# Kernel tuning notes

Measured on AMD Instinct MI355X. Metric: run time of the kernel, lower is better.

## Reference

```python
import jax, jax.numpy as jnp
import numpy as np

B, C, H, W, NH = 4, 96, 256, 256, 4


def setup_inputs() -> dict:
    key = jax.random.key(0)
    ks = jax.random.split(key, 8)
    s = 0.05  # keep pre-activations well-scaled
    return {
        "x": jax.random.normal(ks[0], (B, C, H, W), jnp.float32),
        "ff": jax.random.normal(ks[1], (B, C, H, W), jnp.float32),
        "w_q": jax.random.normal(ks[2], (C, C, 1, 1), jnp.float32) * s,
        "w_kv": jax.random.normal(ks[3], (2 * C, C, 1, 1), jnp.float32) * s,
        "w_q_dw": jax.random.normal(ks[4], (C, 1, 3, 3), jnp.float32) * s,
        "w_kv_dw": jax.random.normal(ks[5], (2 * C, 1, 3, 3), jnp.float32) * s,
        "w_out": jax.random.normal(ks[6], (C, C, 1, 1), jnp.float32) * s,
        "temperature": jnp.ones((NH, 1, 1), jnp.float32),
    }


def _conv1x1(x, w):
    # pointwise conv == channel GEMM; w: [O, I, 1, 1]
    return jnp.einsum('bchw,oc->bohw', x, w[:, :, 0, 0])


def _dwconv3(x, w):
    # depthwise 3x3, padding=1; w: [C, 1, 3, 3]
    return jax.lax.conv_general_dilated(
        x, w, window_strides=(1, 1), padding='SAME',
        feature_group_count=x.shape[1],
        dimension_numbers=('NCHW', 'OIHW', 'NCHW'))


def _l2norm(t, eps=1e-12):
    # L2-normalize along last (HW) axis, torch F.normalize semantics
    n = jnp.sqrt(jnp.sum(t * t, axis=-1, keepdims=True))
    return t / jnp.maximum(n, eps)


def reference(x, ff, w_q, w_kv, w_q_dw, w_kv_dw, w_out, temperature):
    b, c, h, w = x.shape
    q = _dwconv3(_conv1x1(ff, w_q), w_q_dw)          # [B,C,H,W]
    kv = _dwconv3(_conv1x1(x, w_kv), w_kv_dw)        # [B,2C,H,W]
    k, v = jnp.split(kv, 2, axis=1)

    def heads(t):
        return t.reshape(b, NH, c // NH, h * w)       # [B,nh,c,HW]

    q = _l2norm(heads(q))
    k = _l2norm(heads(k))
    v = heads(v)
    # channel-wise (transposed) attention: [B,nh,c,c]
    attn = jax.nn.softmax(jnp.einsum('bhcn,bhdn->bhcd', q, k) * temperature, axis=-1)
    o = jnp.einsum('bhcd,bhdn->bhcn', attn, v).reshape(b, c, h, w)
    return _conv1x1(o, w_out)
```

## Files before the change

### kernel.cpp

```cpp
#include <hip/hip_runtime.h>
#include <hip/hip_bf16.h>
#include <hip/hip_fp16.h>

typedef unsigned int u32;
typedef unsigned short u16;
typedef _Float16 f16;

static constexpr int HWn = 65536;

typedef __attribute__((ext_vector_type(8))) f16 f16x8;
typedef __attribute__((ext_vector_type(2))) f16 f16x2;
typedef __attribute__((ext_vector_type(4))) float f32x4;

__device__ __forceinline__ float h2f(u16 u) {
    union { u16 s; f16 h; } z; z.s = u; return (float)z.h;
}
__device__ __forceinline__ u16 f2h(float f) {
    union { u16 s; f16 h; } z; z.h = (f16)f; return z.s;
}
__device__ __forceinline__ u32 pack2h(float a, float b) {
    union { u32 i; f16 h[2]; } z; z.h[0] = (f16)a; z.h[1] = (f16)b; return z.i;
}
__device__ __forceinline__ float hlo(u32 u) {
    union { u32 i; f16 h[2]; } z; z.i = u; return (float)z.h[0];
}
__device__ __forceinline__ float hhi(u32 u) {
    union { u32 i; f16 h[2]; } z; z.i = u; return (float)z.h[1];
}
__device__ __forceinline__ float sq2h(u32 a) {
    const float l = hlo(a), h = hhi(a);
    return fmaf(l, l, h * h);
}

#if defined(__has_builtin)
#if __has_builtin(__builtin_amdgcn_fdot2)
#define HAS_FDOT2 1
#endif
#endif
__device__ __forceinline__ float fdot2a(u32 a, u32 b, float c) {
#ifdef HAS_FDOT2
    union { u32 i; f16x2 h; } A, B; A.i = a; B.i = b;
    return __builtin_amdgcn_fdot2(A.h, B.h, c, false);
#else
    return fmaf(hlo(a), hlo(b), fmaf(hhi(a), hhi(b), c));
#endif
}

__device__ __forceinline__ int xoff(int px, int icb) {
    return px * 128 + (((icb ^ (px & 7) ^ ((px >> 3) & 7))) << 3);
}

__global__ __launch_bounds__(256) void k_prep_w(
    const float* __restrict__ wq, const float* __restrict__ wkv,
    u16* __restrict__ wf)
{
    const int i = blockIdx.x * 256 + threadIdx.x;
    if (i >= 288 * 96) return;
    const int row = i / 96, ic = i % 96;
    const float w = (row < 96) ? wq[row * 96 + ic] : wkv[(row - 96) * 96 + ic];
    wf[i] = f2h(w);
}

__global__ __launch_bounds__(256, 5) void k_conv_mfma(
    const float* __restrict__ ff, const float* __restrict__ x,
    const u16* __restrict__ wf,
    u16* __restrict__ qpre, u16* __restrict__ kvpre)
{
    const int b = blockIdx.z, sec = blockIdx.y;
    const int px0 = blockIdx.x * 128;
    const int tid = threadIdx.x;

    __shared__ __align__(16) u16 xs[16384];

    const float* src = (sec == 0 ? ff : x) + (size_t)b * 96 * HWn;

    const int icq = (tid >> 4) * 2;
    const int pxs = (tid & 15) * 8;
    #pragma unroll 1
    for (int p = 0; p < 3; ++p) {
        const int ic = p * 32 + icq;
        const float* rp0 = src + (size_t)ic * HWn + px0 + pxs;
        const float* rp1 = rp0 + HWn;
        const float4 a0 = *reinterpret_cast<const float4*>(rp0);
        const float4 a1 = *reinterpret_cast<const float4*>(rp0 + 4);
        const float4 b0 = *reinterpret_cast<const float4*>(rp1);
        const float4 b1 = *reinterpret_cast<const float4*>(rp1 + 4);
        const int icb = ic >> 3, icl = ic & 7;
        const float e0[8] = {a0.x, a0.y, a0.z, a0.w, a1.x, a1.y, a1.z, a1.w};
        const float e1[8] = {b0.x, b0.y, b0.z, b0.w, b1.x, b1.y, b1.z, b1.w};
        #pragma unroll
        for (int j = 0; j < 8; ++j) {
            const int o = xoff(pxs + j, icb) + icl;
            *reinterpret_cast<u32*>(&xs[o]) = pack2h(e0[j], e1[j]);
        }
    }
    __syncthreads();

    const int lane = tid & 63;
    const int wv = tid >> 6;
    const int oc0 = (wv >> 1) * 48;
    const int pxw = (wv & 1) * 64;
    const int lr = lane & 15, lg = lane >> 4;

    const int npass = (sec == 0) ? 1 : 2;
    #pragma unroll 1
    for (int kvs = 0; kvs < npass; ++kvs) {
        const u16* wh = wf + ((sec == 0) ? 0 : (96 + kvs * 96)) * 96;
        u16* dst = (sec == 0) ? (qpre + (size_t)b * 96 * HWn)
                              : (kvpre + (size_t)b * 192 * HWn + (size_t)kvs * 96 * HWn);

        f32x4 acc[3][4];
        #pragma unroll
        for (int m = 0; m < 3; ++m)
            #pragma unroll
            for (int n = 0; n < 4; ++n)
                acc[m][n] = (f32x4){0.f, 0.f, 0.f, 0.f};

        #pragma unroll 1
        for (int kt = 0; kt < 3; ++kt) {
            const int kb = kt * 32;
            f16x8 B[4];
            #pragma unroll
            for (int n = 0; n < 4; ++n)
                B[n] = *(const f16x8*)(xs + xoff(pxw + n * 16 + lr, (kb >> 3) + lg));
            f16x8 A[3];
            #pragma unroll
            for (int m = 0; m < 3; ++m)
                A[m] = *(const f16x8*)(wh + (oc0 + m * 16 + lr) * 96 + kb + lg * 8);
            #pragma unroll
            for (int m = 0; m < 3; ++m)
                #pragma unroll
                for (int n = 0; n < 4; ++n)
                    acc[m][n] = __builtin_amdgcn_mfma_f32_16x16x32_f16(A[m], B[n], acc[m][n], 0, 0, 0);
        }

        #pragma unroll
        for (int m = 0; m < 3; ++m) {
            #pragma unroll
            for (int i = 0; i < 4; ++i) {
                const int oc = oc0 + m * 16 + lg * 4 + i;
                u16* drow = dst + (size_t)oc * HWn + px0;
                #pragma unroll
                for (int n = 0; n < 4; ++n)
                    drow[pxw + n * 16 + lr] = f2h(acc[m][n][i]);
            }
        }
    }
}

__device__ __forceinline__ void row3tap(
    const uint4 m, u32 lv, u32 rv, u32 w01, u32 w2z, float* a)
{
    const u32 P0 = m.x, P1 = m.y, P2 = m.z, P3 = m.w;
    const u32 s0 = (lv >> 16) | (P0 << 16);
    const u32 s1 = (P0 >> 16) | (P1 << 16);
    const u32 s2 = (P1 >> 16) | (P2 << 16);
    const u32 s3 = (P2 >> 16) | (P3 << 16);
    const u32 s4 = (P3 >> 16) | (rv << 16);
    a[0] = fdot2a(w2z, s1, fdot2a(w01, s0, a[0]));
    a[1] = fdot2a(w2z, P1, fdot2a(w01, P0, a[1]));
    a[2] = fdot2a(w2z, s2, fdot2a(w01, s1, a[2]));
    a[3] = fdot2a(w2z, P2, fdot2a(w01, P1, a[3]));
    a[4] = fdot2a(w2z, s3, fdot2a(w01, s2, a[4]));
    a[5] = fdot2a(w2z, P3, fdot2a(w01, P2, a[5]));
    a[6] = fdot2a(w2z, s4, fdot2a(w01, s3, a[6]));
    a[7] = fdot2a(w2z, rv, fdot2a(w01, P3, a[7]));
}

__global__ __launch_bounds__(512) void k_dw_qk(
    const u16* __restrict__ qpre, const u16* __restrict__ kvpre,
    const float* __restrict__ wqdw, const float* __restrict__ wkvdw,
    float* __restrict__ ssq, float* __restrict__ Sg)
{
    const int bid = blockIdx.x;
    const int wg = (bid & 7) * 256 + (bid >> 3);
    const int b = wg >> 9;
    const int rem = wg & 511;
    const int y = rem >> 1;
    const int tx = (rem & 1) * 128;
    const int tid = threadIdx.x;
    const int lane = tid & 63;
    const int pq = tid >> 4;
    const int chunk = tid & 15;
    const int x0l = chunk * 8;
    const int xg = tx + x0l;

    const bool vr0 = (y > 0), vr2 = (y < 255);
    const bool le = (chunk == 0) && (xg > 0);
    const bool re = (chunk == 15) && (xg + 8 < 256);

    __shared__ __align__(16) u16 qs[96][136];
    __shared__ __align__(16) u16 ks[96][136];

    auto addr = [&](int it, const u16*& src, const float*& wp, int& c, int& seg) {
        const int p = it * 32 + pq;
        if (p < 96) { c = p;      src = qpre  + ((size_t)(b * 96 + c)) * HWn;  wp = wqdw  + c * 9; seg = 0; }
        else        { c = p - 96; src = kvpre + ((size_t)(b * 192 + c)) * HWn; wp = wkvdw + c * 9; seg = 1; }
    };
    auto issue = [&](const u16* src, uint4* m, u32* el, u32* er) {
        const uint4 z = make_uint4(0u, 0u, 0u, 0u);
        const u16* r0 = src + (y - 1) * 256 + xg;
        const u16* r1 = r0 + 256;
        const u16* r2 = r1 + 256;
        m[0] = vr0 ? *reinterpret_cast<const uint4*>(r0) : z;
        m[1] = *reinterpret_cast<const uint4*>(r1);
        m[2] = vr2 ? *reinterpret_cast<const uint4*>(r2) : z;
        el[0] = (le && vr0) ? ((u32)r0[-1] << 16) : 0u;  er[0] = (re && vr0) ? (u32)r0[8] : 0u;
        el[1] = le ? ((u32)r1[-1] << 16) : 0u;           er[1] = re ? (u32)r1[8] : 0u;
        el[2] = (le && vr2) ? ((u32)r2[-1] << 16) : 0u;  er[2] = (re && vr2) ? (u32)r2[8] : 0u;
    };

    const u16* srcC; const float* wpC; int cC, segC;
    addr(0, srcC, wpC, cC, segC);
    uint4 mcur[3]; u32 elc[3], erc[3];
    issue(srcC, mcur, elc, erc);

    #pragma unroll 1
    for (int it = 0; it < 6; ++it) {
        const u16* srcN; const float* wpN; int cN, segN;
        uint4 mnx[3]; u32 eln[3], ern[3];
        if (it < 5) {
            addr(it + 1, srcN, wpN, cN, segN);
            issue(srcN, mnx, eln, ern);
        }

        float a[8] = {0.f, 0.f, 0.f, 0.f, 0.f, 0.f, 0.f, 0.f};
        #pragma unroll
        for (int r = 0; r < 3; ++r) {
            const u32 w01 = pack2h(wpC[r * 3 + 0], wpC[r * 3 + 1]);
            const u32 w2z = pack2h(wpC[r * 3 + 2], 0.f);
            const u32 lvn = __shfl((int)mcur[r].w, (lane - 1) & 63);
            const u32 rvn = __shfl((int)mcur[r].x, (lane + 1) & 63);
            const u32 lv = (chunk == 0)  ? elc[r] : lvn;
            const u32 rv = (chunk == 15) ? erc[r] : rvn;
            row3tap(mcur[r], lv, rv, w01, w2z, a);
        }

        const uint4 o = make_uint4(pack2h(a[0], a[1]), pack2h(a[2], a[3]),
                                   pack2h(a[4], a[5]), pack2h(a[6], a[7]));
        if (segC == 0) *reinterpret_cast<uint4*>(&qs[cC][x0l]) = o;
        else           *reinterpret_cast<uint4*>(&ks[cC][x0l]) = o;

        if (it < 5) {
            #pragma unroll
            for (int r = 0; r < 3; ++r) { mcur[r] = mnx[r]; elc[r] = eln[r]; erc[r] = ern[r]; }
            wpC = wpN; cC = cN; segC = segN;
        }
    }
    __syncthreads();

    if (tid < 384) {
        const int half = tid >= 192;
        const int r = tid - half * 192;
        const uint4* rr = reinterpret_cast<const uint4*>(
            (r < 96 ? &qs[r][0] : &ks[r - 96][0]) + half * 64);
        float s = 0.f;
        #pragma unroll
        for (int pch = 0; pch < 8; ++pch) {
            const uint4 a = rr[pch];
            s += sq2h(a.x) + sq2h(a.y) + sq2h(a.z) + sq2h(a.w);
        }
        atomicAdd(ssq + b * 192 + r, s);
    }

    {
        const int w = tid >> 6;
        const int h = w & 3, mt = w >> 2;
        const int lr2 = lane & 15, lg2 = lane >> 4;
        const int ar = h * 24 + min(mt * 16 + lr2, 23);
        f32x4 acc2[2];
        acc2[0] = (f32x4){0.f, 0.f, 0.f, 0.f};
        acc2[1] = (f32x4){0.f, 0.f, 0.f, 0.f};
        #pragma unroll
        for (int ks4 = 0; ks4 < 4; ++ks4) {
            const f16x8 A = *(const f16x8*)(&qs[ar][ks4 * 32 + lg2 * 8]);
            #pragma unroll
            for (int nt = 0; nt < 2; ++nt) {
                const int bc = h * 24 + min(nt * 16 + lr2, 23);
                const f16x8 B = *(const f16x8*)(&ks[bc][ks4 * 32 + lg2 * 8]);
                acc2[nt] = __builtin_amdgcn_mfma_f32_16x16x32_f16(A, B, acc2[nt], 0, 0, 0);
            }
        }
        #pragma unroll
        for (int nt = 0; nt < 2; ++nt) {
            const int col = nt * 16 + lr2;
            #pragma unroll
            for (int reg = 0; reg < 4; ++reg) {
                const int row24 = mt * 16 + lg2 * 4 + reg;
                if (row24 < 24 && col < 24)
                    atomicAdd(Sg + b * 2304 + h * 576 + row24 * 24 + col, acc2[nt][reg]);
            }
        }
    }
}

__global__ __launch_bounds__(512) void k_dw_v(
    const u16* __restrict__ kvpre, const float* __restrict__ wkvdw,
    u16* __restrict__ vout)
{
    const int bid = blockIdx.x;
    const int y = (bid & 7) * 32 + (bid >> 3);
    const int b = blockIdx.y;
    const int tid = threadIdx.x;
    const int lane = tid & 63;
    const int pl = tid >> 5;
    const int chunk = tid & 31;
    const int x0 = chunk * 8;

    const bool vr0 = (y > 0), vr2 = (y < 255);

    auto issue = [&](int it, uint4* m) {
        const int c = it * 16 + pl;
        const u16* src = kvpre + ((size_t)(b * 192 + 96 + c)) * HWn;
        const uint4 z = make_uint4(0u, 0u, 0u, 0u);
        const u16* r0 = src + (y - 1) * 256 + x0;
        m[0] = vr0 ? *reinterpret_cast<const uint4*>(r0) : z;
        m[1] = *reinterpret_cast<const uint4*>(r0 + 256);
        m[2] = vr2 ? *reinterpret_cast<const uint4*>(r0 + 512) : z;
    };

    uint4 mcur[3];
    issue(0, mcur);

    #pragma unroll 1
    for (int it = 0; it < 6; ++it) {
        uint4 mnx[3];
        if (it < 5) issue(it + 1, mnx);

        const int c = it * 16 + pl;
        const float* wp = wkvdw + (96 + c) * 9;

        float a[8] = {0.f, 0.f, 0.f, 0.f, 0.f, 0.f, 0.f, 0.f};
        #pragma unroll
        for (int r = 0; r < 3; ++r) {
            const u32 w01 = pack2h(wp[r * 3 + 0], wp[r * 3 + 1]);
            const u32 w2z = pack2h(wp[r * 3 + 2], 0.f);
            const u32 lvn = __shfl((int)mcur[r].w, (lane - 1) & 63);
            const u32 rvn = __shfl((int)mcur[r].x, (lane + 1) & 63);
            const u32 lv = (chunk == 0)  ? 0u : lvn;
            const u32 rv = (chunk == 31) ? 0u : rvn;
            row3tap(mcur[r], lv, rv, w01, w2z, a);
        }

        const uint4 o = make_uint4(pack2h(a[0], a[1]), pack2h(a[2], a[3]),
                                   pack2h(a[4], a[5]), pack2h(a[6], a[7]));
        *reinterpret_cast<uint4*>(vout + ((size_t)(b * 96 + c)) * HWn + y * 256 + x0) = o;

        if (it < 5) {
            #pragma unroll
            for (int r = 0; r < 3; ++r) mcur[r] = mnx[r];
        }
    }
}

__global__ __launch_bounds__(256) void k_attn_fold(
    const float* __restrict__ ssq, const float* __restrict__ S,
    const float* __restrict__ temp, const float* __restrict__ w_out,
    u16* __restrict__ mf)
{
    const int b = blockIdx.x;
    const int tid = threadIdx.x;
    __shared__ float rq[96], rk[96], att[2304];

    if (tid < 96) {
        rq[tid] = 1.f / fmaxf(sqrtf(ssq[b * 192 + tid]), 1e-12f);
    } else if (tid < 192) {
        const int c = tid - 96;
        rk[c] = 1.f / fmaxf(sqrtf(ssq[b * 192 + 96 + c]), 1e-12f);
    }
    __syncthreads();

    if (tid < 96) {
        const int h = tid / 24, i = tid % 24;
        const float tmp = temp[h];
        const float rqi = rq[h * 24 + i];
        float l[24];
        float m = -1e30f;
        #pragma unroll
        for (int j = 0; j < 24; ++j) {
            l[j] = S[b * 2304 + (h * 24 + i) * 24 + j] * rqi * rk[h * 24 + j] * tmp;
            m = fmaxf(m, l[j]);
        }
        float ssum = 0.f;
        #pragma unroll
        for (int j = 0; j < 24; ++j) { l[j] = expf(l[j] - m); ssum += l[j]; }
        const float inv = 1.f / ssum;
        #pragma unroll
        for (int j = 0; j < 24; ++j) att[(h * 24 + i) * 24 + j] = l[j] * inv;
    }
    __syncthreads();

    for (int k = 0; k < 36; ++k) {
        const int id = k * 256 + tid;
        const int dg = id / 96, oc = id % 96;
        const int h = dg / 24, d24 = dg % 24;
        float s = 0.f;
        #pragma unroll
        for (int i = 0; i < 24; ++i) {
            s += w_out[oc * 96 + h * 24 + i] * att[(h * 24 + i) * 24 + d24];
        }
        mf[b * 9216 + oc * 96 + dg] = f2h(s);
    }
}

__global__ __launch_bounds__(256, 5) void k_out_mfma(
    const u16* __restrict__ v, const u16* __restrict__ mf,
    float* __restrict__ out)
{
    const int b = blockIdx.y;
    const int px0 = blockIdx.x * 128;
    const int tid = threadIdx.x;
    __shared__ __align__(16) u16 xt[16384];

    const u16* vb = v + (size_t)b * 96 * HWn;
    const u16* mh = mf + b * 9216;

    const int icq = (tid >> 4) * 2;
    const int pxs = (tid & 15) * 8;
    #pragma unroll 1
    for (int p = 0; p < 3; ++p) {
        const int dg = p * 32 + icq;
        const uint4 u0 = *reinterpret_cast<const uint4*>(vb + (size_t)dg * HWn + px0 + pxs);
        const uint4 u1 = *reinterpret_cast<const uint4*>(vb + (size_t)(dg + 1) * HWn + px0 + pxs);
        const u32 w0[4] = {u0.x, u0.y, u0.z, u0.w};
        const u32 w1[4] = {u1.x, u1.y, u1.z, u1.w};
        const int icb = dg >> 3, icl = dg & 7;
        #pragma unroll
        for (int j = 0; j < 8; ++j) {
            const u32 lo = (w0[j >> 1] >> ((j & 1) * 16)) & 0xffffu;
            const u32 hi = (w1[j >> 1] >> ((j & 1) * 16)) & 0xffffu;
            const int o = xoff(pxs + j, icb) + icl;
            *reinterpret_cast<u32*>(&xt[o]) = (hi << 16) | lo;
        }
    }
    __syncthreads();

    const int lane = tid & 63;
    const int wv = tid >> 6;
    const int oc0 = (wv >> 1) * 48;
    const int pxw = (wv & 1) * 64;
    const int lr = lane & 15, lg = lane >> 4;

    f32x4 acc[3][4];
    #pragma unroll
    for (int m = 0; m < 3; ++m)
        #pragma unroll
        for (int n = 0; n < 4; ++n)
            acc[m][n] = (f32x4){0.f, 0.f, 0.f, 0.f};

    #pragma unroll 1
    for (int kt = 0; kt < 3; ++kt) {
        const int kb = kt * 32;
        f16x8 B[4];
        #pragma unroll
        for (int n = 0; n < 4; ++n)
            B[n] = *(const f16x8*)(xt + xoff(pxw + n * 16 + lr, (kb >> 3) + lg));
        f16x8 A[3];
        #pragma unroll
        for (int m = 0; m < 3; ++m)
            A[m] = *(const f16x8*)(mh + (oc0 + m * 16 + lr) * 96 + kb + lg * 8);
        #pragma unroll
        for (int m = 0; m < 3; ++m)
            #pragma unroll
            for (int n = 0; n < 4; ++n)
                acc[m][n] = __builtin_amdgcn_mfma_f32_16x16x32_f16(A[m], B[n], acc[m][n], 0, 0, 0);
    }

    #pragma unroll
    for (int m = 0; m < 3; ++m) {
        #pragma unroll
        for (int i = 0; i < 4; ++i) {
            const int oc = oc0 + m * 16 + lg * 4 + i;
            float* drow = out + ((size_t)(b * 96 + oc)) * HWn + px0;
            #pragma unroll
            for (int n = 0; n < 4; ++n)
                drow[pxw + n * 16 + lr] = acc[m][n][i];
        }
    }
}

extern "C" void kernel_launch(void* const* d_in, const int* in_sizes, int n_in,
                              void* d_out, int out_size, void* d_ws, size_t ws_size,
                              hipStream_t stream) {
    (void)in_sizes; (void)n_in; (void)out_size; (void)ws_size;
    const float* x      = (const float*)d_in[0];
    const float* ff     = (const float*)d_in[1];
    const float* w_q    = (const float*)d_in[2];
    const float* w_kv   = (const float*)d_in[3];
    const float* w_q_dw = (const float*)d_in[4];
    const float* w_kv_dw= (const float*)d_in[5];
    const float* w_out  = (const float*)d_in[6];
    const float* temp   = (const float*)d_in[7];
    float* out = (float*)d_out;

    char* ws = (char*)d_ws;
    u16* qpre   = (u16*)(ws);
    u16* kvpre  = (u16*)(ws + 50331648);
    u16* vbuf   = (u16*)(ws + 150994944);
    float* ssq  = (float*)(ws + 201326592);
    float* S    = (float*)(ws + 201329664);
    u16* wf     = (u16*)(ws + 201366528);
    u16* mf     = (u16*)(ws + 201421824);

    hipMemsetAsync(ws + 201326592, 0, 3072 + 36864, stream);

    k_prep_w<<<108, 256, 0, stream>>>(w_q, w_kv, wf);
    k_conv_mfma<<<dim3(512, 2, 4), 256, 0, stream>>>(ff, x, wf, qpre, kvpre);
    k_dw_qk<<<dim3(2048), 512, 0, stream>>>(qpre, kvpre, w_q_dw, w_kv_dw, ssq, S);
    k_dw_v<<<dim3(256, 4), 512, 0, stream>>>(kvpre, w_kv_dw, vbuf);
    k_attn_fold<<<4, 256, 0, stream>>>(ssq, S, temp, w_out, mf);
    k_out_mfma<<<dim3(512, 4), 256, 0, stream>>>(vbuf, mf, out);
}
```

Baseline: 273.0 us.

## Fuse V depthwise conv into output GEMM and pipeline conv loads

The separate depthwise-3x3 kernel for V is removed. Its work now runs inside the output GEMM kernel, which computes the V tile for one half-row directly into LDS (halo pixels come from neighbour-lane shuffles and edge loads) and then does the MFMA with the folded attention/output matrix. This drops the write and reread of the fp16 V intermediate and one kernel launch. Separately, the pointwise conv kernel now handles two 128-pixel tiles per block and prefetches the second tile's global loads while computing the first, at the cost of more registers and lower occupancy (launch bounds 5 to 3).

```diff
diff --git a/kernel.cpp b/kernel.cpp
--- a/kernel.cpp
+++ b/kernel.cpp
@@ -61,91 +61,110 @@
     wf[i] = f2h(w);
 }
 
-__global__ __launch_bounds__(256, 5) void k_conv_mfma(
+__global__ __launch_bounds__(256, 3) void k_conv_mfma(
     const float* __restrict__ ff, const float* __restrict__ x,
     const u16* __restrict__ wf,
     u16* __restrict__ qpre, u16* __restrict__ kvpre)
 {
     const int b = blockIdx.z, sec = blockIdx.y;
-    const int px0 = blockIdx.x * 128;
+    const int pxb = blockIdx.x * 256;
     const int tid = threadIdx.x;
 
     __shared__ __align__(16) u16 xs[16384];
 
     const float* src = (sec == 0 ? ff : x) + (size_t)b * 96 * HWn;
-
     const int icq = (tid >> 4) * 2;
     const int pxs = (tid & 15) * 8;
-    #pragma unroll 1
-    for (int p = 0; p < 3; ++p) {
-        const int ic = p * 32 + icq;
-        const float* rp0 = src + (size_t)ic * HWn + px0 + pxs;
-        const float* rp1 = rp0 + HWn;
-        const float4 a0 = *reinterpret_cast<const float4*>(rp0);
-        const float4 a1 = *reinterpret_cast<const float4*>(rp0 + 4);
-        const float4 b0 = *reinterpret_cast<const float4*>(rp1);
-        const float4 b1 = *reinterpret_cast<const float4*>(rp1 + 4);
-        const int icb = ic >> 3, icl = ic & 7;
-        const float e0[8] = {a0.x, a0.y, a0.z, a0.w, a1.x, a1.y, a1.z, a1.w};
-        const float e1[8] = {b0.x, b0.y, b0.z, b0.w, b1.x, b1.y, b1.z, b1.w};
-        #pragma unroll
-        for (int j = 0; j < 8; ++j) {
-            const int o = xoff(pxs + j, icb) + icl;
-            *reinterpret_cast<u32*>(&xs[o]) = pack2h(e0[j], e1[j]);
-        }
-    }
-    __syncthreads();
-
     const int lane = tid & 63;
     const int wv = tid >> 6;
     const int oc0 = (wv >> 1) * 48;
     const int pxw = (wv & 1) * 64;
     const int lr = lane & 15, lg = lane >> 4;
 
-    const int npass = (sec == 0) ? 1 : 2;
-    #pragma unroll 1
-    for (int kvs = 0; kvs < npass; ++kvs) {
-        const u16* wh = wf + ((sec == 0) ? 0 : (96 + kvs * 96)) * 96;
-        u16* dst = (sec == 0) ? (qpre + (size_t)b * 96 * HWn)
-                              : (kvpre + (size_t)b * 192 * HWn + (size_t)kvs * 96 * HWn);
-
-        f32x4 acc[3][4];
-        #pragma unroll
-        for (int m = 0; m < 3; ++m)
-            #pragma unroll
-            for (int n = 0; n < 4; ++n)
-                acc[m][n] = (f32x4){0.f, 0.f, 0.f, 0.f};
-
+    float4 L[12];
+
+    auto issue = [&](int px0) {
+        #pragma unroll
+        for (int p = 0; p < 3; ++p) {
+            const float* rp0 = src + (size_t)(p * 32 + icq) * HWn + px0 + pxs;
+            const float* rp1 = rp0 + HWn;
+            L[p * 4 + 0] = *reinterpret_cast<const float4*>(rp0);
+            L[p * 4 + 1] = *reinterpret_cast<const float4*>(rp0 + 4);
+            L[p * 4 + 2] = *reinterpret_cast<const float4*>(rp1);
+            L[p * 4 + 3] = *reinterpret_cast<const float4*>(rp1 + 4);
+        }
+    };
+    auto stage = [&]() {
+        #pragma unroll
+        for (int p = 0; p < 3; ++p) {
+            const int ic = p * 32 + icq;
+            const int icb = ic >> 3, icl = ic & 7;
+            const float e0[8] = {L[p*4+0].x, L[p*4+0].y, L[p*4+0].z, L[p*4+0].w,
+                                 L[p*4+1].x, L[p*4+1].y, L[p*4+1].z, L[p*4+1].w};
+            const float e1[8] = {L[p*4+2].x, L[p*4+2].y, L[p*4+2].z, L[p*4+2].w,
+                                 L[p*4+3].x, L[p*4+3].y, L[p*4+3].z, L[p*4+3].w};
+            #pragma unroll
+            for (int j = 0; j < 8; ++j) {
+                const int o = xoff(pxs + j, icb) + icl;
+                *reinterpret_cast<u32*>(&xs[o]) = pack2h(e0[j], e1[j]);
+            }
+        }
+    };
+    auto compute = [&](int px0) {
+        const int npass = (sec == 0) ? 1 : 2;
         #pragma unroll 1
-        for (int kt = 0; kt < 3; ++kt) {
-            const int kb = kt * 32;
-            f16x8 B[4];
-            #pragma unroll
-            for (int n = 0; n < 4; ++n)
-                B[n] = *(const f16x8*)(xs + xoff(pxw + n * 16 + lr, (kb >> 3) + lg));
-            f16x8 A[3];
-            #pragma unroll
-            for (int m = 0; m < 3; ++m)
-                A[m] = *(const f16x8*)(wh + (oc0 + m * 16 + lr) * 96 + kb + lg * 8);
+        for (int kvs = 0; kvs < npass; ++kvs) {
+            const u16* wh = wf + ((sec == 0) ? 0 : (96 + kvs * 96)) * 96;
+            u16* dst = (sec == 0) ? (qpre + (size_t)b * 96 * HWn)
+                                  : (kvpre + (size_t)b * 192 * HWn + (size_t)kvs * 96 * HWn);
+            f32x4 acc[3][4];
             #pragma unroll
             for (int m = 0; m < 3; ++m)
                 #pragma unroll
                 for (int n = 0; n < 4; ++n)
-                    acc[m][n] = __builtin_amdgcn_mfma_f32_16x16x32_f16(A[m], B[n], acc[m][n], 0, 0, 0);
-        }
-
-        #pragma unroll
-        for (int m = 0; m < 3; ++m) {
-            #pragma unroll
-            for (int i = 0; i < 4; ++i) {
-                const int oc = oc0 + m * 16 + lg * 4 + i;
-                u16* drow = dst + (size_t)oc * HWn + px0;
+                    acc[m][n] = (f32x4){0.f, 0.f, 0.f, 0.f};
+
+            #pragma unroll 1
+            for (int kt = 0; kt < 3; ++kt) {
+                const int kb = kt * 32;
+                f16x8 B[4];
                 #pragma unroll
                 for (int n = 0; n < 4; ++n)
-                    drow[pxw + n * 16 + lr] = f2h(acc[m][n][i]);
-            }
-        }
-    }
+                    B[n] = *(const f16x8*)(xs + xoff(pxw + n * 16 + lr, (kb >> 3) + lg));
+                f16x8 A[3];
+                #pragma unroll
+                for (int m = 0; m < 3; ++m)
+                    A[m] = *(const f16x8*)(wh + (oc0 + m * 16 + lr) * 96 + kb + lg * 8);
+                #pragma unroll
+                for (int m = 0; m < 3; ++m)
+                    #pragma unroll
+                    for (int n = 0; n < 4; ++n)
+                        acc[m][n] = __builtin_amdgcn_mfma_f32_16x16x32_f16(A[m], B[n], acc[m][n], 0, 0, 0);
+            }
+
+            #pragma unroll
+            for (int m = 0; m < 3; ++m) {
+                #pragma unroll
+                for (int i = 0; i < 4; ++i) {
+                    const int oc = oc0 + m * 16 + lg * 4 + i;
+                    u16* drow = dst + (size_t)oc * HWn + px0;
+                    #pragma unroll
+                    for (int n = 0; n < 4; ++n)
+                        drow[pxw + n * 16 + lr] = f2h(acc[m][n][i]);
+                }
+            }
+        }
+    };
+
+    issue(pxb);
+    stage();
+    __syncthreads();
+    issue(pxb + 128);
+    compute(pxb);
+    __syncthreads();
+    stage();
+    __syncthreads();
+    compute(pxb + 128);
 }
 
 __device__ __forceinline__ void row3tap(
@@ -294,65 +313,6 @@
     }
 }
 
-__global__ __launch_bounds__(512) void k_dw_v(
-    const u16* __restrict__ kvpre, const float* __restrict__ wkvdw,
-    u16* __restrict__ vout)
-{
-    const int bid = blockIdx.x;
-    const int y = (bid & 7) * 32 + (bid >> 3);
-    const int b = blockIdx.y;
-    const int tid = threadIdx.x;
-    const int lane = tid & 63;
-    const int pl = tid >> 5;
-    const int chunk = tid & 31;
-    const int x0 = chunk * 8;
-
-    const bool vr0 = (y > 0), vr2 = (y < 255);
-
-    auto issue = [&](int it, uint4* m) {
-        const int c = it * 16 + pl;
-        const u16* src = kvpre + ((size_t)(b * 192 + 96 + c)) * HWn;
-        const uint4 z = make_uint4(0u, 0u, 0u, 0u);
-        const u16* r0 = src + (y - 1) * 256 + x0;
-        m[0] = vr0 ? *reinterpret_cast<const uint4*>(r0) : z;
-        m[1] = *reinterpret_cast<const uint4*>(r0 + 256);
-        m[2] = vr2 ? *reinterpret_cast<const uint4*>(r0 + 512) : z;
-    };
-
-    uint4 mcur[3];
-    issue(0, mcur);
-
-    #pragma unroll 1
-    for (int it = 0; it < 6; ++it) {
-        uint4 mnx[3];
-        if (it < 5) issue(it + 1, mnx);
-
-        const int c = it * 16 + pl;
-        const float* wp = wkvdw + (96 + c) * 9;
-
-        float a[8] = {0.f, 0.f, 0.f, 0.f, 0.f, 0.f, 0.f, 0.f};
-        #pragma unroll
-        for (int r = 0; r < 3; ++r) {
-            const u32 w01 = pack2h(wp[r * 3 + 0], wp[r * 3 + 1]);
-            const u32 w2z = pack2h(wp[r * 3 + 2], 0.f);
-            const u32 lvn = __shfl((int)mcur[r].w, (lane - 1) & 63);
-            const u32 rvn = __shfl((int)mcur[r].x, (lane + 1) & 63);
-            const u32 lv = (chunk == 0)  ? 0u : lvn;
-            const u32 rv = (chunk == 31) ? 0u : rvn;
-            row3tap(mcur[r], lv, rv, w01, w2z, a);
-        }
-
-        const uint4 o = make_uint4(pack2h(a[0], a[1]), pack2h(a[2], a[3]),
-                                   pack2h(a[4], a[5]), pack2h(a[6], a[7]));
-        *reinterpret_cast<uint4*>(vout + ((size_t)(b * 96 + c)) * HWn + y * 256 + x0) = o;
-
-        if (it < 5) {
-            #pragma unroll
-            for (int r = 0; r < 3; ++r) mcur[r] = mnx[r];
-        }
-    }
-}
-
 __global__ __launch_bounds__(256) void k_attn_fold(
     const float* __restrict__ ssq, const float* __restrict__ S,
     const float* __restrict__ temp, const float* __restrict__ w_out,
@@ -403,39 +363,102 @@
     }
 }
 
-__global__ __launch_bounds__(256, 5) void k_out_mfma(
-    const u16* __restrict__ v, const u16* __restrict__ mf,
-    float* __restrict__ out)
+__global__ __launch_bounds__(256, 4) void k_v_out(
+    const u16* __restrict__ kvpre, const float* __restrict__ wkvdw,
+    const u16* __restrict__ mf, float* __restrict__ out)
 {
-    const int b = blockIdx.y;
-    const int px0 = blockIdx.x * 128;
+    const int bid = blockIdx.x;
+    const int wg = (bid & 7) * 256 + (bid >> 3);
+    const int b = wg >> 9;
+    const int rem = wg & 511;
+    const int y = rem >> 1;
+    const int tx = (rem & 1) * 128;
     const int tid = threadIdx.x;
+    const int lane = tid & 63;
+    const int slot = tid >> 4;
+    const int chunk = tid & 15;
+    const int x0l = chunk * 8;
+    const int xg = tx + x0l;
+
+    const bool vr0 = (y > 0), vr2 = (y < 255);
+    const bool le = (chunk == 0) && (xg > 0);
+    const bool re = (chunk == 15) && (xg + 8 < 256);
+
     __shared__ __align__(16) u16 xt[16384];
 
-    const u16* vb = v + (size_t)b * 96 * HWn;
+    auto issue = [&](int it, uint4* m0, uint4* m1, u32* e0l, u32* e0r, u32* e1l, u32* e1r) {
+        const int dg = (it * 16 + slot) * 2;
+        const u16* s0 = kvpre + ((size_t)(b * 192 + 96 + dg)) * HWn + (y - 1) * 256 + xg;
+        const u16* s1 = s0 + HWn;
+        const uint4 z = make_uint4(0u, 0u, 0u, 0u);
+        m0[0] = vr0 ? *reinterpret_cast<const uint4*>(s0)       : z;
+        m0[1] =       *reinterpret_cast<const uint4*>(s0 + 256);
+        m0[2] = vr2 ? *reinterpret_cast<const uint4*>(s0 + 512) : z;
+        m1[0] = vr0 ? *reinterpret_cast<const uint4*>(s1)       : z;
+        m1[1] =       *reinterpret_cast<const uint4*>(s1 + 256);
+        m1[2] = vr2 ? *reinterpret_cast<const uint4*>(s1 + 512) : z;
+        e0l[0] = (le && vr0) ? ((u32)s0[-1] << 16) : 0u;   e0r[0] = (re && vr0) ? (u32)s0[8] : 0u;
+        e0l[1] = le ? ((u32)s0[255] << 16) : 0u;           e0r[1] = re ? (u32)s0[264] : 0u;
+        e0l[2] = (le && vr2) ? ((u32)s0[511] << 16) : 0u;  e0r[2] = (re && vr2) ? (u32)s0[520] : 0u;
+        e1l[0] = (le && vr0) ? ((u32)s1[-1] << 16) : 0u;   e1r[0] = (re && vr0) ? (u32)s1[8] : 0u;
+        e1l[1] = le ? ((u32)s1[255] << 16) : 0u;           e1r[1] = re ? (u32)s1[264] : 0u;
+        e1l[2] = (le && vr2) ? ((u32)s1[511] << 16) : 0u;  e1r[2] = (re && vr2) ? (u32)s1[520] : 0u;
+    };
+
+    uint4 m0c[3], m1c[3]; u32 e0lc[3], e0rc[3], e1lc[3], e1rc[3];
+    issue(0, m0c, m1c, e0lc, e0rc, e1lc, e1rc);
+
+    #pragma unroll 1
+    for (int it = 0; it < 3; ++it) {
+        uint4 m0n[3], m1n[3]; u32 e0ln[3], e0rn[3], e1ln[3], e1rn[3];
+        if (it < 2) issue(it + 1, m0n, m1n, e0ln, e0rn, e1ln, e1rn);
+
+        const int dg = (it * 16 + slot) * 2;
+        const float* wp0 = wkvdw + (96 + dg) * 9;
+        const float* wp1 = wp0 + 9;
+
+        float a0[8] = {0.f, 0.f, 0.f, 0.f, 0.f, 0.f, 0.f, 0.f};
+        float a1[8] = {0.f, 0.f, 0.f, 0.f, 0.f, 0.f, 0.f, 0.f};
+        #pragma unroll
+        for (int r = 0; r < 3; ++r) {
+            {
+                const u32 w01 = pack2h(wp0[r * 3 + 0], wp0[r * 3 + 1]);
+                const u32 w2z = pack2h(wp0[r * 3 + 2], 0.f);
+                const u32 lvn = __shfl((int)m0c[r].w, (lane - 1) & 63);
+                const u32 rvn = __shfl((int)m0c[r].x, (lane + 1) & 63);
+                const u32 lv = (chunk == 0)  ? e0lc[r] : lvn;
+                const u32 rv = (chunk == 15) ? e0rc[r] : rvn;
+                row3tap(m0c[r], lv, rv, w01, w2z, a0);
+            }
+            {
+                const u32 w01 = pack2h(wp1[r * 3 + 0], wp1[r * 3 + 1]);
+                const u32 w2z = pack2h(wp1[r * 3 + 2], 0.f);
+                const u32 lvn = __shfl((int)m1c[r].w, (lane - 1) & 63);
+                const u32 rvn = __shfl((int)m1c[r].x, (lane + 1) & 63);
+                const u32 lv = (chunk == 0)  ? e1lc[r] : lvn;
+                const u32 rv = (chunk == 15) ? e1rc[r] : rvn;
+                row3tap(m1c[r], lv, rv, w01, w2z, a1);
+            }
+        }
+
+        const int icb = dg >> 3, icl = dg & 7;
+        #pragma unroll
+        for (int j = 0; j < 8; ++j) {
+            *reinterpret_cast<u32*>(&xt[xoff(x0l + j, icb) + icl]) = pack2h(a0[j], a1[j]);
+        }
+
+        if (it < 2) {
+            #pragma unroll
+            for (int r = 0; r < 3; ++r) {
+                m0c[r] = m0n[r]; m1c[r] = m1n[r];
+                e0lc[r] = e0ln[r]; e0rc[r] = e0rn[r];
+                e1lc[r] = e1ln[r]; e1rc[r] = e1rn[r];
+            }
+        }
+    }
+    __syncthreads();
+
     const u16* mh = mf + b * 9216;
-
-    const int icq = (tid >> 4) * 2;
-    const int pxs = (tid & 15) * 8;
-    #pragma unroll 1
-    for (int p = 0; p < 3; ++p) {
-        const int dg = p * 32 + icq;
-        const uint4 u0 = *reinterpret_cast<const uint4*>(vb + (size_t)dg * HWn + px0 + pxs);
-        const uint4 u1 = *reinterpret_cast<const uint4*>(vb + (size_t)(dg + 1) * HWn + px0 + pxs);
-        const u32 w0[4] = {u0.x, u0.y, u0.z, u0.w};
-        const u32 w1[4] = {u1.x, u1.y, u1.z, u1.w};
-        const int icb = dg >> 3, icl = dg & 7;
-        #pragma unroll
-        for (int j = 0; j < 8; ++j) {
-            const u32 lo = (w0[j >> 1] >> ((j & 1) * 16)) & 0xffffu;
-            const u32 hi = (w1[j >> 1] >> ((j & 1) * 16)) & 0xffffu;
-            const int o = xoff(pxs + j, icb) + icl;
-            *reinterpret_cast<u32*>(&xt[o]) = (hi << 16) | lo;
-        }
-    }
-    __syncthreads();
-
-    const int lane = tid & 63;
     const int wv = tid >> 6;
     const int oc0 = (wv >> 1) * 48;
     const int pxw = (wv & 1) * 64;
@@ -471,7 +494,7 @@
         #pragma unroll
         for (int i = 0; i < 4; ++i) {
             const int oc = oc0 + m * 16 + lg * 4 + i;
-            float* drow = out + ((size_t)(b * 96 + oc)) * HWn + px0;
+            float* drow = out + ((size_t)(b * 96 + oc)) * HWn + y * 256 + tx;
             #pragma unroll
             for (int n = 0; n < 4; ++n)
                 drow[pxw + n * 16 + lr] = acc[m][n][i];
@@ -496,18 +519,16 @@
     char* ws = (char*)d_ws;
     u16* qpre   = (u16*)(ws);
     u16* kvpre  = (u16*)(ws + 50331648);
-    u16* vbuf   = (u16*)(ws + 150994944);
-    float* ssq  = (float*)(ws + 201326592);
-    float* S    = (float*)(ws + 201329664);
-    u16* wf     = (u16*)(ws + 201366528);
-    u16* mf     = (u16*)(ws + 201421824);
-
-    hipMemsetAsync(ws + 201326592, 0, 3072 + 36864, stream);
+    float* ssq  = (float*)(ws + 150994944);
+    float* S    = (float*)(ws + 150998016);
+    u16* wf     = (u16*)(ws + 151034880);
+    u16* mf     = (u16*)(ws + 151090176);
+
+    hipMemsetAsync(ws + 150994944, 0, 3072 + 36864, stream);
 
     k_prep_w<<<108, 256, 0, stream>>>(w_q, w_kv, wf);
-    k_conv_mfma<<<dim3(512, 2, 4), 256, 0, stream>>>(ff, x, wf, qpre, kvpre);
+    k_conv_mfma<<<dim3(256, 2, 4), 256, 0, stream>>>(ff, x, wf, qpre, kvpre);
     k_dw_qk<<<dim3(2048), 512, 0, stream>>>(qpre, kvpre, w_q_dw, w_kv_dw, ssq, S);
-    k_dw_v<<<dim3(256, 4), 512, 0, stream>>>(kvpre, w_kv_dw, vbuf);
     k_attn_fold<<<4, 256, 0, stream>>>(ssq, S, temp, w_out, mf);
-    k_out_mfma<<<dim3(512, 4), 256, 0, stream>>>(vbuf, mf, out);
-}
+    k_v_out<<<dim3(2048), 256, 0, stream>>>(kvpre, w_kv_dw, mf, out);
+}
```

After: 257.0 us. 5.8% less time.
